# Kernel tuning notes

Measured on AMD Instinct MI355X. Metric: run time of the kernel, lower is better.

Reference implementation:

```python
import jax, jax.numpy as jnp
import numpy as np

EPS = 1e-6

def _feature_map(x):
    # elu(x) + 1
    return jax.nn.elu(x) + 1.0

def setup_inputs() -> dict:
    key = jax.random.key(0)
    kq, kk, kv = jax.random.split(key, 3)
    N, L, S, H, D = 4, 8192, 8192, 8, 64
    queries = jax.random.normal(kq, (N, L, H, D), dtype=jnp.float32)
    keys = jax.random.normal(kk, (N, S, H, D), dtype=jnp.float32)
    values = jax.random.normal(kv, (N, S, H, D), dtype=jnp.float32)
    return {"queries": queries, "keys": keys, "values": values}

def reference(queries, keys, values):
    # queries: [N,L,H,D], keys/values: [N,S,H,D]
    Q = _feature_map(queries)
    K = _feature_map(keys)
    v_length = values.shape[1]
    v = values / v_length
    # KV = sum_s K[n,s,h,d] * v[n,s,h,e] -> [N,H,D,E]
    KV = jnp.einsum("nshd,nshe->nhde", K, v)
    # Z = 1 / (Q . sum_s K + eps) -> [N,L,H]
    K_sum = jnp.sum(K, axis=1)  # [N,H,D]
    Z = 1.0 / (jnp.einsum("nlhd,nhd->nlh", Q, K_sum) + EPS)
    # out = (Q @ KV) * Z * v_length -> [N,L,H,E]
    out = jnp.einsum("nlhd,nhde,nlh->nlhe", Q, KV, Z) * v_length
    return out
```

## Files before the change

kernel.cpp:

```cpp
#include <hip/hip_runtime.h>
#include <cstdint>

#define N_ 4
#define L_ 8192
#define S_ 8192
#define H_ 8
#define D_ 64
#define E_ 64
#define HD_ 512
#define NH_ 32
#define EPS_ 1e-6f
#define TS_ 32

typedef unsigned int u32;
typedef unsigned short u16;
typedef __attribute__((ext_vector_type(4))) float f32x4;
typedef __attribute__((ext_vector_type(8))) __bf16 bf16x8;

__device__ __forceinline__ float elu1(float x) {
  return x > 0.0f ? x + 1.0f : __expf(x);
}
__device__ __forceinline__ u32 cvtpk(float a, float b) {
  u32 r;
  asm("v_cvt_pk_bf16_f32 %0, %1, %2" : "=v"(r) : "v"(a), "v"(b));
  return r;
}
__device__ __forceinline__ f32x4 mfma16(bf16x8 a, bf16x8 b, f32x4 c) {
  return __builtin_amdgcn_mfma_f32_16x16x32_bf16(a, b, c, 0, 0, 0);
}

__global__ __launch_bounds__(512, 8) void p1_kv(const float* __restrict__ keys,
                                                const float* __restrict__ values,
                                                float* __restrict__ pkv,
                                                float* __restrict__ pks,
                                                int tiles) {
  const int chunk = blockIdx.x, h = blockIdx.y, n = blockIdx.z;
  const int tid = threadIdx.x, w = tid >> 6, lane = tid & 63;
  const int m = lane & 15, kb = lane >> 4;
  const int srow = tid >> 4, scol4 = (tid & 15) * 4;
  __shared__ u16 lds[16384];
  char* base = (char*)lds;

  const int dd = w & 3, ee0 = (w >> 2) * 2;
  const int Ra = dd * 16 + m;
  const int aoff = (Ra * 128 + kb * 16) ^ (((Ra >> 1) & 7) << 4);
  const int Rb0 = ee0 * 16 + m, Rb1 = Rb0 + 16;
  const int b0off = ((Rb0 * 128 + kb * 16) ^ (((Rb0 >> 1) & 7) << 4)) + 8192;
  const int b1off = ((Rb1 * 128 + kb * 16) ^ (((Rb1 >> 1) & 7) << 4)) + 8192;
  int wo[4];
  #pragma unroll
  for (int j = 0; j < 4; ++j) {
    int R = scol4 + j;
    wo[j] = (R * 128 + (srow >> 1) * 4) ^ (((R >> 1) & 7) << 4);
  }
  const bool wr = !(srow & 1);

  const float* Kb_ = keys   + (size_t)n * S_ * HD_ + h * D_;
  const float* Vb_ = values + (size_t)n * S_ * HD_ + h * D_;
  u32 goff = (u32)((chunk * tiles * TS_ + srow) * HD_ + scol4);

  f32x4 acc0 = {0.f, 0.f, 0.f, 0.f}, acc1 = {0.f, 0.f, 0.f, 0.f};
  float4 kss = make_float4(0.f, 0.f, 0.f, 0.f);

  float4 kA = *(const float4*)(Kb_ + goff);
  float4 vA = *(const float4*)(Vb_ + goff);
  float4 kB, vB;

#define STAGE(k4, v4, BUF)                                                     \
  {                                                                            \
    float4 f;                                                                  \
    f.x = elu1(k4.x); f.y = elu1(k4.y); f.z = elu1(k4.z); f.w = elu1(k4.w);    \
    kss.x += f.x; kss.y += f.y; kss.z += f.z; kss.w += f.w;                    \
    u32 kl = cvtpk(f.x, f.y), kh = cvtpk(f.z, f.w);                            \
    u32 vl = cvtpk(v4.x, v4.y), vh = cvtpk(v4.z, v4.w);                        \
    u32 pkl = (u32)__shfl_xor((int)kl, 16, 64);                                \
    u32 pkh = (u32)__shfl_xor((int)kh, 16, 64);                                \
    u32 pvl = (u32)__shfl_xor((int)vl, 16, 64);                                \
    u32 pvh = (u32)__shfl_xor((int)vh, 16, 64);                                \
    if (wr) {                                                                  \
      *(u32*)(base + (BUF) + wo[0]) = __builtin_amdgcn_perm(pkl, kl, 0x05040100u); \
      *(u32*)(base + (BUF) + wo[1]) = __builtin_amdgcn_perm(pkl, kl, 0x07060302u); \
      *(u32*)(base + (BUF) + wo[2]) = __builtin_amdgcn_perm(pkh, kh, 0x05040100u); \
      *(u32*)(base + (BUF) + wo[3]) = __builtin_amdgcn_perm(pkh, kh, 0x07060302u); \
      *(u32*)(base + (BUF) + 8192 + wo[0]) = __builtin_amdgcn_perm(pvl, vl, 0x05040100u); \
      *(u32*)(base + (BUF) + 8192 + wo[1]) = __builtin_amdgcn_perm(pvl, vl, 0x07060302u); \
      *(u32*)(base + (BUF) + 8192 + wo[2]) = __builtin_amdgcn_perm(pvh, vh, 0x05040100u); \
      *(u32*)(base + (BUF) + 8192 + wo[3]) = __builtin_amdgcn_perm(pvh, vh, 0x07060302u); \
    }                                                                          \
  }

#define COMPUTE(BUF)                                                           \
  {                                                                            \
    uint4 ar  = *(const uint4*)(base + (BUF) + aoff);                          \
    uint4 b0r = *(const uint4*)(base + (BUF) + b0off);                         \
    uint4 b1r = *(const uint4*)(base + (BUF) + b1off);                         \
    bf16x8 av = __builtin_bit_cast(bf16x8, ar);                                \
    acc0 = mfma16(av, __builtin_bit_cast(bf16x8, b0r), acc0);                  \
    acc1 = mfma16(av, __builtin_bit_cast(bf16x8, b1r), acc1);                  \
  }

  #pragma unroll 1
  for (int t = 0; t < tiles; t += 2) {
    STAGE(kA, vA, 0)
    { goff += TS_ * HD_;
      kB = *(const float4*)(Kb_ + goff);
      vB = *(const float4*)(Vb_ + goff); }
    asm volatile("s_waitcnt lgkmcnt(0)" ::: "memory");
    __builtin_amdgcn_s_barrier();
    COMPUTE(0)
    STAGE(kB, vB, 16384)
    if (t + 2 < tiles) { goff += TS_ * HD_;
      kA = *(const float4*)(Kb_ + goff);
      vA = *(const float4*)(Vb_ + goff); }
    asm volatile("s_waitcnt lgkmcnt(0)" ::: "memory");
    __builtin_amdgcn_s_barrier();
    COMPUTE(16384)
  }
#undef STAGE
#undef COMPUTE

  float* pkvb = pkv + ((size_t)chunk * NH_ + (size_t)(n * H_ + h)) * (D_ * E_);
  #pragma unroll
  for (int r = 0; r < 4; ++r) {
    pkvb[(dd * 16 + kb * 4 + r) * 64 + ee0 * 16 + m]       = acc0[r];
    pkvb[(dd * 16 + kb * 4 + r) * 64 + (ee0 + 1) * 16 + m] = acc1[r];
  }

  __syncthreads();
  float* sc = (float*)lds;
  *(float4*)(sc + srow * 64 + scol4) = kss;
  __syncthreads();
  if (tid < 64) {
    float s = 0.f;
    #pragma unroll
    for (int r = 0; r < 32; ++r) s += sc[r * 64 + tid];
    pks[((size_t)chunk * NH_ + (size_t)(n * H_ + h)) * 64 + tid] = s;
  }
}

__global__ __launch_bounds__(256) void reduce_kv(const float* __restrict__ pkv,
                                                 const float* __restrict__ pks,
                                                 u16* __restrict__ kvt5, int C) {
  const int nh = blockIdx.x, tid = threadIdx.x;
  __shared__ float lds[64 * 65];
  float acc[16];
  #pragma unroll
  for (int k = 0; k < 16; ++k) acc[k] = 0.f;
  #pragma unroll 1
  for (int c = 0; c < C; ++c) {
    const float* p = pkv + ((size_t)c * NH_ + nh) * 4096;
    #pragma unroll
    for (int j = 0; j < 4; ++j) {
      float4 f = *(const float4*)(p + j * 1024 + tid * 4);
      acc[j * 4 + 0] += f.x; acc[j * 4 + 1] += f.y;
      acc[j * 4 + 2] += f.z; acc[j * 4 + 3] += f.w;
    }
  }
  #pragma unroll
  for (int j = 0; j < 4; ++j)
    #pragma unroll
    for (int k2 = 0; k2 < 4; ++k2)
      lds[(j * 16 + (tid >> 4)) * 65 + (tid & 15) * 4 + k2] = acc[j * 4 + k2];
  __syncthreads();
  {
    const int e = tid >> 2, d0 = (tid & 3) * 16;
    u32 pk8[8];
    #pragma unroll
    for (int q = 0; q < 8; ++q)
      pk8[q] = cvtpk(lds[(d0 + 2 * q) * 65 + e], lds[(d0 + 2 * q + 1) * 65 + e]);
    u16* dst = kvt5 + (size_t)nh * (80 * 64) + e * 64 + d0;
    *(uint4*)(dst)     = make_uint4(pk8[0], pk8[1], pk8[2], pk8[3]);
    *(uint4*)(dst + 8) = make_uint4(pk8[4], pk8[5], pk8[6], pk8[7]);
  }
  if (tid < 64) {
    float s = 0.f;
    #pragma unroll 1
    for (int c = 0; c < C; ++c) s += pks[((size_t)c * NH_ + nh) * 64 + tid];
    kvt5[(size_t)nh * (80 * 64) + 64 * 64 + tid] = (u16)(cvtpk(s, 0.f) & 0xffffu);
  }
  {
    u32* z = (u32*)(kvt5 + (size_t)nh * (80 * 64) + 65 * 64);
    for (int i = tid; i < 480; i += 256) z[i] = 0u;
  }
}

__global__ __launch_bounds__(256, 4) void p2_out(const float* __restrict__ queries,
                                                 const u16* __restrict__ kvt5,
                                                 float* __restrict__ out) {
  const int lt = blockIdx.x, h = blockIdx.y, n = blockIdx.z;
  const int tid = threadIdx.x, w = tid >> 6, lane = tid & 63;
  const int m = lane & 15, kb = lane >> 4;
  const int nh = n * H_ + h;
  const u16* kp = kvt5 + (size_t)nh * (80 * 64);
  uint4 B[5][2];
  #pragma unroll
  for (int ee = 0; ee < 5; ++ee)
    #pragma unroll
    for (int ks = 0; ks < 2; ++ks)
      B[ee][ks] = *(const uint4*)(kp + (ee * 16 + m) * 64 + ks * 32 + kb * 8);

  #pragma unroll 1
  for (int rt = 0; rt < 2; ++rt) {
    const int rowbase = lt * 128 + rt * 64 + w * 16;
    const float* qp = queries + ((size_t)(n * L_ + rowbase + m) * H_ + h) * D_;
    float4 qa = *(const float4*)(qp + kb * 8);
    float4 qb_ = *(const float4*)(qp + kb * 8 + 4);
    float4 qc = *(const float4*)(qp + 32 + kb * 8);
    float4 qd = *(const float4*)(qp + 32 + kb * 8 + 4);
    uint4 a0r, a1r;
    a0r.x = cvtpk(elu1(qa.x), elu1(qa.y));  a0r.y = cvtpk(elu1(qa.z), elu1(qa.w));
    a0r.z = cvtpk(elu1(qb_.x), elu1(qb_.y)); a0r.w = cvtpk(elu1(qb_.z), elu1(qb_.w));
    a1r.x = cvtpk(elu1(qc.x), elu1(qc.y));  a1r.y = cvtpk(elu1(qc.z), elu1(qc.w));
    a1r.z = cvtpk(elu1(qd.x), elu1(qd.y));  a1r.w = cvtpk(elu1(qd.z), elu1(qd.w));
    bf16x8 a0 = __builtin_bit_cast(bf16x8, a0r);
    bf16x8 a1 = __builtin_bit_cast(bf16x8, a1r);
    f32x4 acc[5];
    #pragma unroll
    for (int ee = 0; ee < 5; ++ee) {
      acc[ee] = f32x4{0.f, 0.f, 0.f, 0.f};
      acc[ee] = mfma16(a0, __builtin_bit_cast(bf16x8, B[ee][0]), acc[ee]);
      acc[ee] = mfma16(a1, __builtin_bit_cast(bf16x8, B[ee][1]), acc[ee]);
    }
    float z[4];
    #pragma unroll
    for (int r = 0; r < 4; ++r) {
      float dn = __shfl(acc[4][r], lane & 48, 64);
#if __has_builtin(__builtin_amdgcn_rcpf)
      z[r] = __builtin_amdgcn_rcpf(dn + EPS_);
#else
      z[r] = 1.0f / (dn + EPS_);
#endif
    }
    float* ob = out + ((size_t)(n * L_ + rowbase) * H_ + h) * E_;
    #pragma unroll
    for (int ee = 0; ee < 4; ++ee)
      #pragma unroll
      for (int r = 0; r < 4; ++r)
        ob[(size_t)(kb * 4 + r) * (H_ * E_) + ee * 16 + m] = acc[ee][r] * z[r];
  }
}

extern "C" void kernel_launch(void* const* d_in, const int* in_sizes, int n_in,
                              void* d_out, int out_size, void* d_ws, size_t ws_size,
                              hipStream_t stream) {
  const float* q = (const float*)d_in[0];
  const float* k = (const float*)d_in[1];
  const float* v = (const float*)d_in[2];
  float* outp = (float*)d_out;

  int C = 32;
  while (C > 1) {
    size_t need = ((size_t)C * NH_ * (4096 + 64)) * sizeof(float)
                + (size_t)NH_ * 80 * 64 * sizeof(u16);
    if (need <= ws_size) break;
    C >>= 1;
  }
  float* pkv = (float*)d_ws;
  float* pks = pkv + (size_t)C * NH_ * 4096;
  u16* kvt5 = (u16*)(pks + (size_t)C * NH_ * 64);
  const int tiles = S_ / (C * TS_);

  hipLaunchKernelGGL(p1_kv, dim3(C, H_, N_), dim3(512), 0, stream, k, v, pkv, pks, tiles);
  hipLaunchKernelGGL(reduce_kv, dim3(NH_), dim3(256), 0, stream, pkv, pks, kvt5, C);
  hipLaunchKernelGGL(p2_out, dim3(L_ / 128, H_, N_), dim3(256), 0, stream, q, kvt5, outp);
}
```

Before: 86.02 us.

## Split K/V loading across half-blocks and double tile depth to 64 rows

The KV partial kernel now uses the first 256 threads to load keys and the other 256 to load values. Each thread loads four rows and packs a column of four bf16 values directly with one 8-byte LDS write, which removes the cross-lane shuffles and perm instructions. The tile depth doubles to 64 rows, so each barrier feeds four MFMAs per wave instead of two and there are half as many synchronisations. The cost is more registers per thread, K-only divergence for the ELU work, and a host-side tiles count that must match the new tile size.

```diff
diff --git a/kernel.cpp b/kernel.cpp
--- a/kernel.cpp
+++ b/kernel.cpp
@@ -10,7 +10,7 @@
 #define HD_ 512
 #define NH_ 32
 #define EPS_ 1e-6f
-#define TS_ 32
+#define TS_ 64
 
 typedef unsigned int u32;
 typedef unsigned short u16;
@@ -37,87 +37,92 @@
   const int chunk = blockIdx.x, h = blockIdx.y, n = blockIdx.z;
   const int tid = threadIdx.x, w = tid >> 6, lane = tid & 63;
   const int m = lane & 15, kb = lane >> 4;
-  const int srow = tid >> 4, scol4 = (tid & 15) * 4;
   __shared__ u16 lds[16384];
   char* base = (char*)lds;
 
+  const bool isK = (tid < 256);
+  const int c4 = tid & 15;
+  const int sgrp = (tid >> 4) & 15;
+  const int regionOff = isK ? 0 : 8192;
+  int wo[4];
+  #pragma unroll
+  for (int j = 0; j < 4; ++j) {
+    const int R = c4 * 4 + j;
+    wo[j] = regionOff + R * 128 + ((sgrp * 8) ^ (((R >> 1) & 7) << 4));
+  }
+
   const int dd = w & 3, ee0 = (w >> 2) * 2;
   const int Ra = dd * 16 + m;
-  const int aoff = (Ra * 128 + kb * 16) ^ (((Ra >> 1) & 7) << 4);
+  const int swA = ((Ra >> 1) & 7) << 4;
+  const int aoff0 = Ra * 128 + ((kb * 16) ^ swA);
+  const int aoff1 = Ra * 128 + ((64 + kb * 16) ^ swA);
   const int Rb0 = ee0 * 16 + m, Rb1 = Rb0 + 16;
-  const int b0off = ((Rb0 * 128 + kb * 16) ^ (((Rb0 >> 1) & 7) << 4)) + 8192;
-  const int b1off = ((Rb1 * 128 + kb * 16) ^ (((Rb1 >> 1) & 7) << 4)) + 8192;
-  int wo[4];
-  #pragma unroll
-  for (int j = 0; j < 4; ++j) {
-    int R = scol4 + j;
-    wo[j] = (R * 128 + (srow >> 1) * 4) ^ (((R >> 1) & 7) << 4);
-  }
-  const bool wr = !(srow & 1);
-
-  const float* Kb_ = keys   + (size_t)n * S_ * HD_ + h * D_;
-  const float* Vb_ = values + (size_t)n * S_ * HD_ + h * D_;
-  u32 goff = (u32)((chunk * tiles * TS_ + srow) * HD_ + scol4);
+  const int swB0 = ((Rb0 >> 1) & 7) << 4, swB1 = ((Rb1 >> 1) & 7) << 4;
+  const int boff00 = 8192 + Rb0 * 128 + ((kb * 16) ^ swB0);
+  const int boff01 = 8192 + Rb0 * 128 + ((64 + kb * 16) ^ swB0);
+  const int boff10 = 8192 + Rb1 * 128 + ((kb * 16) ^ swB1);
+  const int boff11 = 8192 + Rb1 * 128 + ((64 + kb * 16) ^ swB1);
+
+  const float* gsrc = (isK ? keys : values) + (size_t)n * S_ * HD_ + h * D_;
+  u32 goff = (u32)((chunk * tiles * TS_ + sgrp * 4) * HD_ + c4 * 4);
 
   f32x4 acc0 = {0.f, 0.f, 0.f, 0.f}, acc1 = {0.f, 0.f, 0.f, 0.f};
   float4 kss = make_float4(0.f, 0.f, 0.f, 0.f);
 
-  float4 kA = *(const float4*)(Kb_ + goff);
-  float4 vA = *(const float4*)(Vb_ + goff);
-  float4 kB, vB;
-
-#define STAGE(k4, v4, BUF)                                                     \
-  {                                                                            \
-    float4 f;                                                                  \
-    f.x = elu1(k4.x); f.y = elu1(k4.y); f.z = elu1(k4.z); f.w = elu1(k4.w);    \
-    kss.x += f.x; kss.y += f.y; kss.z += f.z; kss.w += f.w;                    \
-    u32 kl = cvtpk(f.x, f.y), kh = cvtpk(f.z, f.w);                            \
-    u32 vl = cvtpk(v4.x, v4.y), vh = cvtpk(v4.z, v4.w);                        \
-    u32 pkl = (u32)__shfl_xor((int)kl, 16, 64);                                \
-    u32 pkh = (u32)__shfl_xor((int)kh, 16, 64);                                \
-    u32 pvl = (u32)__shfl_xor((int)vl, 16, 64);                                \
-    u32 pvh = (u32)__shfl_xor((int)vh, 16, 64);                                \
-    if (wr) {                                                                  \
-      *(u32*)(base + (BUF) + wo[0]) = __builtin_amdgcn_perm(pkl, kl, 0x05040100u); \
-      *(u32*)(base + (BUF) + wo[1]) = __builtin_amdgcn_perm(pkl, kl, 0x07060302u); \
-      *(u32*)(base + (BUF) + wo[2]) = __builtin_amdgcn_perm(pkh, kh, 0x05040100u); \
-      *(u32*)(base + (BUF) + wo[3]) = __builtin_amdgcn_perm(pkh, kh, 0x07060302u); \
-      *(u32*)(base + (BUF) + 8192 + wo[0]) = __builtin_amdgcn_perm(pvl, vl, 0x05040100u); \
-      *(u32*)(base + (BUF) + 8192 + wo[1]) = __builtin_amdgcn_perm(pvl, vl, 0x07060302u); \
-      *(u32*)(base + (BUF) + 8192 + wo[2]) = __builtin_amdgcn_perm(pvh, vh, 0x05040100u); \
-      *(u32*)(base + (BUF) + 8192 + wo[3]) = __builtin_amdgcn_perm(pvh, vh, 0x07060302u); \
-    }                                                                          \
-  }
-
-#define COMPUTE(BUF)                                                           \
-  {                                                                            \
-    uint4 ar  = *(const uint4*)(base + (BUF) + aoff);                          \
-    uint4 b0r = *(const uint4*)(base + (BUF) + b0off);                         \
-    uint4 b1r = *(const uint4*)(base + (BUF) + b1off);                         \
-    bf16x8 av = __builtin_bit_cast(bf16x8, ar);                                \
-    acc0 = mfma16(av, __builtin_bit_cast(bf16x8, b0r), acc0);                  \
-    acc1 = mfma16(av, __builtin_bit_cast(bf16x8, b1r), acc1);                  \
-  }
+  float4 r0 = *(const float4*)(gsrc + goff);
+  float4 r1 = *(const float4*)(gsrc + goff + HD_);
+  float4 r2 = *(const float4*)(gsrc + goff + 2 * HD_);
+  float4 r3 = *(const float4*)(gsrc + goff + 3 * HD_);
+
+#define COLW(BUF, j, F0, F1, F2, F3)                                           \
+  { u32 lo_ = cvtpk(F0, F1), hi_ = cvtpk(F2, F3);                              \
+    *(uint2*)(base + (BUF) + wo[j]) = make_uint2(lo_, hi_); }
 
   #pragma unroll 1
-  for (int t = 0; t < tiles; t += 2) {
-    STAGE(kA, vA, 0)
-    { goff += TS_ * HD_;
-      kB = *(const float4*)(Kb_ + goff);
-      vB = *(const float4*)(Vb_ + goff); }
+  for (int t = 0; t < tiles; ++t) {
+    const int BUF = (t & 1) * 16384;
+    {
+      float4 f0 = r0, f1 = r1, f2 = r2, f3 = r3;
+      if (isK) {
+        f0.x = elu1(f0.x); f0.y = elu1(f0.y); f0.z = elu1(f0.z); f0.w = elu1(f0.w);
+        f1.x = elu1(f1.x); f1.y = elu1(f1.y); f1.z = elu1(f1.z); f1.w = elu1(f1.w);
+        f2.x = elu1(f2.x); f2.y = elu1(f2.y); f2.z = elu1(f2.z); f2.w = elu1(f2.w);
+        f3.x = elu1(f3.x); f3.y = elu1(f3.y); f3.z = elu1(f3.z); f3.w = elu1(f3.w);
+        kss.x += f0.x + f1.x + f2.x + f3.x;
+        kss.y += f0.y + f1.y + f2.y + f3.y;
+        kss.z += f0.z + f1.z + f2.z + f3.z;
+        kss.w += f0.w + f1.w + f2.w + f3.w;
+      }
+      COLW(BUF, 0, f0.x, f1.x, f2.x, f3.x)
+      COLW(BUF, 1, f0.y, f1.y, f2.y, f3.y)
+      COLW(BUF, 2, f0.z, f1.z, f2.z, f3.z)
+      COLW(BUF, 3, f0.w, f1.w, f2.w, f3.w)
+    }
+    if (t + 1 < tiles) {
+      goff += TS_ * HD_;
+      r0 = *(const float4*)(gsrc + goff);
+      r1 = *(const float4*)(gsrc + goff + HD_);
+      r2 = *(const float4*)(gsrc + goff + 2 * HD_);
+      r3 = *(const float4*)(gsrc + goff + 3 * HD_);
+    }
     asm volatile("s_waitcnt lgkmcnt(0)" ::: "memory");
     __builtin_amdgcn_s_barrier();
-    COMPUTE(0)
-    STAGE(kB, vB, 16384)
-    if (t + 2 < tiles) { goff += TS_ * HD_;
-      kA = *(const float4*)(Kb_ + goff);
-      vA = *(const float4*)(Vb_ + goff); }
-    asm volatile("s_waitcnt lgkmcnt(0)" ::: "memory");
-    __builtin_amdgcn_s_barrier();
-    COMPUTE(16384)
-  }
-#undef STAGE
-#undef COMPUTE
+    {
+      uint4 a0r = *(const uint4*)(base + BUF + aoff0);
+      uint4 a1r = *(const uint4*)(base + BUF + aoff1);
+      uint4 b00 = *(const uint4*)(base + BUF + boff00);
+      uint4 b01 = *(const uint4*)(base + BUF + boff01);
+      uint4 b10 = *(const uint4*)(base + BUF + boff10);
+      uint4 b11 = *(const uint4*)(base + BUF + boff11);
+      bf16x8 a0 = __builtin_bit_cast(bf16x8, a0r);
+      bf16x8 a1 = __builtin_bit_cast(bf16x8, a1r);
+      acc0 = mfma16(a0, __builtin_bit_cast(bf16x8, b00), acc0);
+      acc0 = mfma16(a1, __builtin_bit_cast(bf16x8, b01), acc0);
+      acc1 = mfma16(a0, __builtin_bit_cast(bf16x8, b10), acc1);
+      acc1 = mfma16(a1, __builtin_bit_cast(bf16x8, b11), acc1);
+    }
+  }
+#undef COLW
 
   float* pkvb = pkv + ((size_t)chunk * NH_ + (size_t)(n * H_ + h)) * (D_ * E_);
   #pragma unroll
@@ -128,12 +133,12 @@
 
   __syncthreads();
   float* sc = (float*)lds;
-  *(float4*)(sc + srow * 64 + scol4) = kss;
+  if (isK) *(float4*)(sc + sgrp * 64 + c4 * 4) = kss;
   __syncthreads();
   if (tid < 64) {
     float s = 0.f;
     #pragma unroll
-    for (int r = 0; r < 32; ++r) s += sc[r * 64 + tid];
+    for (int r = 0; r < 16; ++r) s += sc[r * 64 + tid];
     pks[((size_t)chunk * NH_ + (size_t)(n * H_ + h)) * 64 + tid] = s;
   }
 }
```

Measured after the change: 111.6 us. 29.8% more time.
